# Performance work log

Measured on AMD Instinct MI355X. Metric: run time of the kernel, lower is better.

## Reference

```python
import jax, jax.numpy as jnp
import numpy as np

B, IN, H = 4096, 512, 1024
ALPHA, RHO = 0.001, 0.05

def setup_inputs() -> dict:
    key = jax.random.key(0)
    ks = jax.random.split(key, 9)
    inp = jax.random.normal(ks[0], (B, IN), dtype=jnp.float32)
    time = jax.random.uniform(ks[1], (B, 1), dtype=jnp.float32) * 100.0
    hx = jax.random.normal(ks[2], (B, H), dtype=jnp.float32)
    cx = jax.random.normal(ks[3], (B, H), dtype=jnp.float32)
    # params (match torch init scales loosely)
    Wxh_w = jax.random.normal(ks[4], (4 * H, IN), dtype=jnp.float32) / np.sqrt(IN)
    Wxh_b = jnp.zeros((4 * H,), dtype=jnp.float32)
    Whh_w = jax.random.normal(ks[5], (4 * H, H), dtype=jnp.float32) / np.sqrt(H)
    tau = jax.random.normal(ks[6], (H,), dtype=jnp.float32) * 0.5 + 5.0
    s = jax.random.uniform(ks[7], (H,), dtype=jnp.float32) * tau
    alpha = jnp.array([ALPHA], dtype=jnp.float32)
    rho = jnp.array([RHO], dtype=jnp.float32)
    return {"input": inp, "time": time, "hx": hx, "cx": cx,
            "Wxh_w": Wxh_w, "Wxh_b": Wxh_b, "Whh_w": Whh_w,
            "tau": tau, "s": s, "alpha": alpha, "rho": rho}

def _time_gate(time, s, tau, alpha, rho):
    # phi: [B, H] (time [B,1] broadcast against s/tau [H])
    phi = jnp.fmod(time - s, tau) / tau
    k = jnp.where(phi < rho / 2.0, 2.0 * phi / rho,
        jnp.where(phi < rho, 2.0 - 2.0 * phi / rho, alpha * phi))
    # computed under torch.no_grad() in the original
    return jax.lax.stop_gradient(k)

def reference(input, time, hx, cx, Wxh_w, Wxh_b, Whh_w, tau, s, alpha, rho):
    gates = input @ Wxh_w.T + Wxh_b + hx @ Whh_w.T  # [B, 4H]
    i, f, g, o = jnp.split(gates, 4, axis=1)
    k = _time_gate(time, s, tau, alpha, rho)
    ft = jax.nn.sigmoid(f + 1.0 - k)
    it = jax.nn.sigmoid(i) * k
    gt = jnp.tanh(g) * k
    ot = jax.nn.sigmoid(o) * k
    cy = ft * cx + it * gt
    hy = ot * jnp.tanh(cy)
    return (hy, cy)
```

## Files before the change

### kernel.cpp

```cpp
#include <hip/hip_runtime.h>

#define AS1 __attribute__((address_space(1)))
#define AS3 __attribute__((address_space(3)))

typedef _Float16 half_t;
typedef __attribute__((ext_vector_type(8))) _Float16 f16x8;
typedef __attribute__((ext_vector_type(4))) float f32x4;

static constexpr int Bsz = 4096;
static constexpr int INs = 512;
static constexpr int Hs  = 1024;
static constexpr int BM  = 128;
static constexpr int BH  = 32;
static constexpr int BK  = 64;
static constexpr int NIT = INs / BK + Hs / BK;

static constexpr size_t XN  = (size_t)Bsz * INs;
static constexpr size_t HXN = (size_t)Bsz * Hs;
static constexpr size_t WXN = (size_t)4 * Hs * INs;
static constexpr size_t WHN = (size_t)4 * Hs * Hs;
static constexpr size_t OFF_X  = 0;
static constexpr size_t OFF_HX = XN;
static constexpr size_t OFF_WX = XN + HXN;
static constexpr size_t OFF_WH = XN + HXN + WXN;
static constexpr size_t TOT    = XN + HXN + WXN + WHN;

__device__ __forceinline__ float sigm(float x) {
  return 1.0f / (1.0f + __expf(-x));
}
__device__ __forceinline__ float tanh_fast(float x) {
  const float e = __expf(2.0f * x);
  return 1.0f - 2.0f / (e + 1.0f);
}

__global__ __launch_bounds__(256)
void cvt_kernel(const float* __restrict__ x, const float* __restrict__ hx,
                const float* __restrict__ wx, const float* __restrict__ wh,
                half_t* __restrict__ ws) {
  const size_t cid = (size_t)blockIdx.x * 256 + threadIdx.x;
  const size_t e = cid * 8;
  const float* src; size_t off;
  if (e < OFF_HX)      { src = x;  off = e - OFF_X; }
  else if (e < OFF_WX) { src = hx; off = e - OFF_HX; }
  else if (e < OFF_WH) { src = wx; off = e - OFF_WX; }
  else                 { src = wh; off = e - OFF_WH; }
  const f32x4 a = *(const f32x4*)(src + off);
  const f32x4 b = *(const f32x4*)(src + off + 4);
  f16x8 o;
  o[0]=(half_t)a[0]; o[1]=(half_t)a[1]; o[2]=(half_t)a[2]; o[3]=(half_t)a[3];
  o[4]=(half_t)b[0]; o[5]=(half_t)b[1]; o[6]=(half_t)b[2]; o[7]=(half_t)b[3];
  *(f16x8*)(ws + e) = o;
}

__global__ __launch_bounds__(256, 4)
void plstm_gemm(const half_t* __restrict__ xin,
                const half_t* __restrict__ hxp,
                const float* __restrict__ cxp,
                const half_t* __restrict__ wxh,
                const float* __restrict__ biasp,
                const half_t* __restrict__ whh,
                const float* __restrict__ timep,
                const float* __restrict__ taup,
                const float* __restrict__ sp,
                const float* __restrict__ alphap,
                const float* __restrict__ rhop,
                float* __restrict__ outp)
{
  __shared__ half_t As[BM * BK];
  __shared__ half_t Bs[BM * BK];

  const int tid  = threadIdx.x;
  const int w    = tid >> 6;
  const int lane = tid & 63;
  const int l15  = lane & 15;
  const int grp  = lane >> 4;
  const int wr   = w >> 1;
  const int wc   = w & 1;

  const int m0 = blockIdx.x * BM;
  const int h0 = blockIdx.y * BH;

  f32x4 acc[4][4] = {};

  const int ldr = tid >> 3;
  const int ldc = tid & 7;

  for (int it = 0; it < NIT; ++it) {
    const bool p1 = it >= INs / BK;
    const half_t* Ap = p1 ? hxp : xin;
    const half_t* Wp = p1 ? whh : wxh;
    const int Ka = p1 ? Hs : INs;
    const int k0 = (p1 ? (it - INs / BK) : it) * BK;
    #pragma unroll
    for (int i = 0; i < 4; ++i) {
      const int e    = i * 32 + ldr;
      const int gc8  = ldc ^ (e & 7);
      const int wrow = ((e >> 4) & 3) * Hs + h0 + ((e >> 6) << 4) + (e & 15);
      const half_t* ga = Ap + (size_t)(m0 + e) * Ka + (k0 + gc8 * 8);
      __builtin_amdgcn_global_load_lds((AS1 void*)ga,
                                       (AS3 void*)(As + (e * 8 + ldc) * 8), 16, 0, 0);
      const half_t* gw = Wp + (size_t)wrow * Ka + (k0 + gc8 * 8);
      __builtin_amdgcn_global_load_lds((AS1 void*)gw,
                                       (AS3 void*)(Bs + (e * 8 + ldc) * 8), 16, 0, 0);
    }
    __syncthreads();

    #pragma unroll
    for (int kk = 0; kk < 2; ++kk) {
      const int c8x = kk * 4 + grp;
      f16x8 af[4], bfr[4];
      #pragma unroll
      for (int mt = 0; mt < 4; ++mt) {
        const int e = wr * 64 + mt * 16 + l15;
        af[mt] = *(const f16x8*)(As + (e * 8 + (c8x ^ (l15 & 7))) * 8);
      }
      #pragma unroll
      for (int nt = 0; nt < 4; ++nt) {
        const int e = wc * 64 + nt * 16 + l15;
        bfr[nt] = *(const f16x8*)(Bs + (e * 8 + (c8x ^ (l15 & 7))) * 8);
      }
      #pragma unroll
      for (int mt = 0; mt < 4; ++mt)
        #pragma unroll
        for (int nt = 0; nt < 4; ++nt)
          acc[mt][nt] = __builtin_amdgcn_mfma_f32_16x16x32_f16(
              af[mt], bfr[nt], acc[mt][nt], 0, 0, 0);
    }
    __syncthreads();
  }

  const int h = h0 + wc * 16 + l15;
  const float bi  = biasp[h];
  const float bfv = biasp[Hs + h];
  const float bg  = biasp[2 * Hs + h];
  const float bo  = biasp[3 * Hs + h];
  const float sv = sp[h], tauv = taup[h];
  const float alphav = alphap[0], rhov = rhop[0], rh = 0.5f * rhov;

  #pragma unroll
  for (int mt = 0; mt < 4; ++mt) {
    #pragma unroll
    for (int r = 0; r < 4; ++r) {
      const int brow = m0 + wr * 64 + mt * 16 + grp * 4 + r;
      const float tv = timep[brow];
      const float phi = fmodf(tv - sv, tauv) / tauv;
      float kv;
      if (phi < rh)        kv = (2.0f * phi) / rhov;
      else if (phi < rhov) kv = 2.0f - (2.0f * phi) / rhov;
      else                 kv = alphav * phi;

      const float iv = acc[mt][0][r] + bi;
      const float fv = acc[mt][1][r] + bfv;
      const float gv = acc[mt][2][r] + bg;
      const float ov = acc[mt][3][r] + bo;
      const float cxv = cxp[(size_t)brow * Hs + h];
      const float ft = sigm(fv + 1.0f - kv);
      const float it2 = sigm(iv) * kv;
      const float gt = tanh_fast(gv) * kv;
      const float ot = sigm(ov) * kv;
      const float cy = ft * cxv + it2 * gt;
      const float hy = ot * tanh_fast(cy);

      outp[(size_t)brow * Hs + h] = hy;
      outp[(size_t)Bsz * Hs + (size_t)brow * Hs + h] = cy;
    }
  }
}

__global__ __launch_bounds__(256, 3)
void plstm_gemm_f32(const float* __restrict__ xin, const float* __restrict__ timep,
                    const float* __restrict__ hxp, const float* __restrict__ cxp,
                    const float* __restrict__ wxh, const float* __restrict__ biasp,
                    const float* __restrict__ whh, const float* __restrict__ taup,
                    const float* __restrict__ sp, const float* __restrict__ alphap,
                    const float* __restrict__ rhop, float* __restrict__ outp)
{
  __shared__ half_t As[BM * BK];
  __shared__ half_t Bs[BM * BK];

  const int tid  = threadIdx.x;
  const int w    = tid >> 6;
  const int lane = tid & 63;
  const int l15  = lane & 15;
  const int grp  = lane >> 4;
  const int wr   = w >> 1;
  const int wc   = w & 1;

  const int m0 = blockIdx.x * BM;
  const int h0 = blockIdx.y * BH;

  f32x4 acc[4][4] = {};
  const int ldr = tid >> 3;
  const int ldc = tid & 7;

  for (int it = 0; it < NIT; ++it) {
    const bool p1 = it >= INs / BK;
    const float* Ap = p1 ? hxp : xin;
    const float* Wp = p1 ? whh : wxh;
    const int Ka = p1 ? Hs : INs;
    const int k0 = (p1 ? (it - INs / BK) : it) * BK;
    #pragma unroll
    for (int i = 0; i < 4; ++i) {
      const int e    = i * 32 + ldr;
      const int gc8  = ldc ^ (e & 7);
      const int wrow = ((e >> 4) & 3) * Hs + h0 + ((e >> 6) << 4) + (e & 15);
      const float* ga = Ap + (size_t)(m0 + e) * Ka + (k0 + gc8 * 8);
      const f32x4 a0 = *(const f32x4*)ga, a1 = *(const f32x4*)(ga + 4);
      f16x8 pa;
      pa[0]=(half_t)a0[0]; pa[1]=(half_t)a0[1]; pa[2]=(half_t)a0[2]; pa[3]=(half_t)a0[3];
      pa[4]=(half_t)a1[0]; pa[5]=(half_t)a1[1]; pa[6]=(half_t)a1[2]; pa[7]=(half_t)a1[3];
      *(f16x8*)(As + (e * 8 + ldc) * 8) = pa;
      const float* gw = Wp + (size_t)wrow * Ka + (k0 + gc8 * 8);
      const f32x4 b0 = *(const f32x4*)gw, b1 = *(const f32x4*)(gw + 4);
      f16x8 pb;
      pb[0]=(half_t)b0[0]; pb[1]=(half_t)b0[1]; pb[2]=(half_t)b0[2]; pb[3]=(half_t)b0[3];
      pb[4]=(half_t)b1[0]; pb[5]=(half_t)b1[1]; pb[6]=(half_t)b1[2]; pb[7]=(half_t)b1[3];
      *(f16x8*)(Bs + (e * 8 + ldc) * 8) = pb;
    }
    __syncthreads();
    #pragma unroll
    for (int kk = 0; kk < 2; ++kk) {
      const int c8x = kk * 4 + grp;
      f16x8 af[4], bfr[4];
      #pragma unroll
      for (int mt = 0; mt < 4; ++mt) {
        const int e = wr * 64 + mt * 16 + l15;
        af[mt] = *(const f16x8*)(As + (e * 8 + (c8x ^ (l15 & 7))) * 8);
      }
      #pragma unroll
      for (int nt = 0; nt < 4; ++nt) {
        const int e = wc * 64 + nt * 16 + l15;
        bfr[nt] = *(const f16x8*)(Bs + (e * 8 + (c8x ^ (l15 & 7))) * 8);
      }
      #pragma unroll
      for (int mt = 0; mt < 4; ++mt)
        #pragma unroll
        for (int nt = 0; nt < 4; ++nt)
          acc[mt][nt] = __builtin_amdgcn_mfma_f32_16x16x32_f16(
              af[mt], bfr[nt], acc[mt][nt], 0, 0, 0);
    }
    __syncthreads();
  }

  const int h = h0 + wc * 16 + l15;
  const float bi  = biasp[h];
  const float bfv = biasp[Hs + h];
  const float bg  = biasp[2 * Hs + h];
  const float bo  = biasp[3 * Hs + h];
  const float sv = sp[h], tauv = taup[h];
  const float alphav = alphap[0], rhov = rhop[0], rh = 0.5f * rhov;

  #pragma unroll
  for (int mt = 0; mt < 4; ++mt) {
    #pragma unroll
    for (int r = 0; r < 4; ++r) {
      const int brow = m0 + wr * 64 + mt * 16 + grp * 4 + r;
      const float tv = timep[brow];
      const float phi = fmodf(tv - sv, tauv) / tauv;
      float kv;
      if (phi < rh)        kv = (2.0f * phi) / rhov;
      else if (phi < rhov) kv = 2.0f - (2.0f * phi) / rhov;
      else                 kv = alphav * phi;
      const float iv = acc[mt][0][r] + bi;
      const float fv = acc[mt][1][r] + bfv;
      const float gv = acc[mt][2][r] + bg;
      const float ov = acc[mt][3][r] + bo;
      const float cxv = cxp[(size_t)brow * Hs + h];
      const float ft = sigm(fv + 1.0f - kv);
      const float it2 = sigm(iv) * kv;
      const float gt = tanh_fast(gv) * kv;
      const float ot = sigm(ov) * kv;
      const float cy = ft * cxv + it2 * gt;
      const float hy = ot * tanh_fast(cy);
      outp[(size_t)brow * Hs + h] = hy;
      outp[(size_t)Bsz * Hs + (size_t)brow * Hs + h] = cy;
    }
  }
}

extern "C" void kernel_launch(void* const* d_in, const int* in_sizes, int n_in,
                              void* d_out, int out_size, void* d_ws, size_t ws_size,
                              hipStream_t stream) {
  (void)in_sizes; (void)n_in; (void)out_size;
  const float* xin   = (const float*)d_in[0];
  const float* timep = (const float*)d_in[1];
  const float* hxp   = (const float*)d_in[2];
  const float* cxp   = (const float*)d_in[3];
  const float* wxh   = (const float*)d_in[4];
  const float* biasp = (const float*)d_in[5];
  const float* whh   = (const float*)d_in[6];
  const float* taup  = (const float*)d_in[7];
  const float* sp    = (const float*)d_in[8];
  const float* alphap= (const float*)d_in[9];
  const float* rhop  = (const float*)d_in[10];
  float* outp = (float*)d_out;

  dim3 grid(Bsz / BM, Hs / BH);
  if (ws_size >= TOT * sizeof(half_t)) {
    half_t* ws = (half_t*)d_ws;
    cvt_kernel<<<(int)(TOT / 8 / 256), 256, 0, stream>>>(xin, hxp, wxh, whh, ws);
    plstm_gemm<<<grid, 256, 0, stream>>>(
        ws + OFF_X, ws + OFF_HX, cxp, ws + OFF_WX, biasp, ws + OFF_WH,
        timep, taup, sp, alphap, rhop, outp);
  } else {
    plstm_gemm_f32<<<grid, 256, 0, stream>>>(
        xin, timep, hxp, cxp, wxh, biasp, whh,
        taup, sp, alphap, rhop, outp);
  }
}
```

Before: 193.5 us.

## Enlarge fp16 GEMM tile to 256x256 with double-buffered 8-wave pipelined schedule

Replaces the single-buffered 128x128-tile fp16 GEMM with a 256-row by 256-gate tile run by 512 threads. LDS is double-buffered and next-tile global_load_lds staging is interleaved with MFMA quadrants through explicit barriers, waitcnt and s_setprio phases. The aim is to overlap global loads with matrix math and raise arithmetic intensity per block. The risks are higher register pressure from the 8x4 accumulators, fewer blocks in flight, and correctness depending on the hand-placed vmcnt counts.

```diff
diff --git a/kernel.cpp b/kernel.cpp
--- a/kernel.cpp
+++ b/kernel.cpp
@@ -10,10 +10,11 @@
 static constexpr int Bsz = 4096;
 static constexpr int INs = 512;
 static constexpr int Hs  = 1024;
-static constexpr int BM  = 128;
-static constexpr int BH  = 32;
 static constexpr int BK  = 64;
 static constexpr int NIT = INs / BK + Hs / BK;
+
+static constexpr int BM  = 256;
+static constexpr int BHh = 64;
 
 static constexpr size_t XN  = (size_t)Bsz * INs;
 static constexpr size_t HXN = (size_t)Bsz * Hs;
@@ -52,7 +53,75 @@
   *(f16x8*)(ws + e) = o;
 }
 
-__global__ __launch_bounds__(256, 4)
+struct KS { const half_t* A; const half_t* W; int Ka; int k0; };
+
+
+#define STAGE_A(dst, s, mh) do { \
+  _Pragma("unroll") \
+  for (int rr = 0; rr < 2; ++rr) { \
+    const int e_ = rr * 128 + (mh) * 64 + j; \
+    const int gc8_ = ldc ^ (e_ & 7); \
+    const half_t* ga_ = (s).A + (size_t)(m0 + e_) * (s).Ka + ((s).k0 + gc8_ * 8); \
+    __builtin_amdgcn_global_load_lds((AS1 void*)ga_, \
+        (AS3 void*)((dst) + (e_ * 8 + ldc) * 8), 16, 0, 0); \
+  } } while (0)
+
+#define STAGE_B(dst, s, nh) do { \
+  _Pragma("unroll") \
+  for (int rr = 0; rr < 2; ++rr) { \
+    const int e_ = rr * 128 + ((j >> 5) << 6) + (nh) * 32 + (j & 31); \
+    const int gc8_ = ldc ^ (e_ & 7); \
+    const int wrow_ = ((e_ >> 4) & 3) * Hs + h0 + ((e_ >> 6) << 4) + (e_ & 15); \
+    const half_t* gw_ = (s).W + (size_t)wrow_ * (s).Ka + ((s).k0 + gc8_ * 8); \
+    __builtin_amdgcn_global_load_lds((AS1 void*)gw_, \
+        (AS3 void*)((dst) + (e_ * 8 + ldc) * 8), 16, 0, 0); \
+  } } while (0)
+
+#define READ_A(d, base, mh) do { \
+  _Pragma("unroll") \
+  for (int m_ = 0; m_ < 4; ++m_) { \
+    const int e_ = wr * 128 + (mh) * 64 + m_ * 16 + l15; \
+    _Pragma("unroll") \
+    for (int kk_ = 0; kk_ < 2; ++kk_) \
+      d[m_][kk_] = *(const f16x8*)((base) + (e_ * 8 + ((kk_ * 4 + grp) ^ (l15 & 7))) * 8); \
+  } } while (0)
+
+#define READ_B(d, base, nh) do { \
+  _Pragma("unroll") \
+  for (int n_ = 0; n_ < 2; ++n_) { \
+    const int e_ = wcn * 64 + (nh) * 32 + n_ * 16 + l15; \
+    _Pragma("unroll") \
+    for (int kk_ = 0; kk_ < 2; ++kk_) \
+      d[n_][kk_] = *(const f16x8*)((base) + (e_ * 8 + ((kk_ * 4 + grp) ^ (l15 & 7))) * 8); \
+  } } while (0)
+
+#define QUAD(mh, nh, A_, B_) do { \
+  _Pragma("unroll") \
+  for (int m_ = 0; m_ < 4; ++m_) \
+    _Pragma("unroll") \
+    for (int n_ = 0; n_ < 2; ++n_) \
+      _Pragma("unroll") \
+      for (int kk_ = 0; kk_ < 2; ++kk_) \
+        acc[(mh) * 4 + m_][(nh) * 2 + n_] = __builtin_amdgcn_mfma_f32_16x16x32_f16( \
+            A_[m_][kk_], B_[n_][kk_], acc[(mh) * 4 + m_][(nh) * 2 + n_], 0, 0, 0); \
+  } while (0)
+
+#define PH_MID() do { \
+  __builtin_amdgcn_s_barrier(); \
+  asm volatile("s_waitcnt lgkmcnt(0)" ::: "memory"); \
+  __builtin_amdgcn_sched_barrier(0); \
+  __builtin_amdgcn_s_setprio(1); } while (0)
+
+#define PH_END() do { \
+  __builtin_amdgcn_s_setprio(0); \
+  __builtin_amdgcn_s_barrier(); } while (0)
+
+#define PH_END_VM() do { \
+  __builtin_amdgcn_s_setprio(0); \
+  asm volatile("s_waitcnt vmcnt(4)" ::: "memory"); \
+  __builtin_amdgcn_s_barrier(); } while (0)
+
+__global__ __launch_bounds__(512, 2)
 void plstm_gemm(const half_t* __restrict__ xin,
                 const half_t* __restrict__ hxp,
                 const float* __restrict__ cxp,
@@ -66,70 +135,76 @@
                 const float* __restrict__ rhop,
                 float* __restrict__ outp)
 {
-  __shared__ half_t As[BM * BK];
-  __shared__ half_t Bs[BM * BK];
+  __shared__ half_t As[2][BM * BK];
+  __shared__ half_t Bs[2][BM * BK];
 
   const int tid  = threadIdx.x;
   const int w    = tid >> 6;
   const int lane = tid & 63;
   const int l15  = lane & 15;
   const int grp  = lane >> 4;
-  const int wr   = w >> 1;
-  const int wc   = w & 1;
+  const int wr   = w >> 2;
+  const int wcn  = w & 3;
 
   const int m0 = blockIdx.x * BM;
-  const int h0 = blockIdx.y * BH;
-
-  f32x4 acc[4][4] = {};
-
-  const int ldr = tid >> 3;
+  const int h0 = blockIdx.y * BHh;
+
+  const int j   = tid >> 3;
   const int ldc = tid & 7;
 
-  for (int it = 0; it < NIT; ++it) {
-    const bool p1 = it >= INs / BK;
-    const half_t* Ap = p1 ? hxp : xin;
-    const half_t* Wp = p1 ? whh : wxh;
-    const int Ka = p1 ? Hs : INs;
-    const int k0 = (p1 ? (it - INs / BK) : it) * BK;
-    #pragma unroll
-    for (int i = 0; i < 4; ++i) {
-      const int e    = i * 32 + ldr;
-      const int gc8  = ldc ^ (e & 7);
-      const int wrow = ((e >> 4) & 3) * Hs + h0 + ((e >> 6) << 4) + (e & 15);
-      const half_t* ga = Ap + (size_t)(m0 + e) * Ka + (k0 + gc8 * 8);
-      __builtin_amdgcn_global_load_lds((AS1 void*)ga,
-                                       (AS3 void*)(As + (e * 8 + ldc) * 8), 16, 0, 0);
-      const half_t* gw = Wp + (size_t)wrow * Ka + (k0 + gc8 * 8);
-      __builtin_amdgcn_global_load_lds((AS1 void*)gw,
-                                       (AS3 void*)(Bs + (e * 8 + ldc) * 8), 16, 0, 0);
-    }
-    __syncthreads();
-
-    #pragma unroll
-    for (int kk = 0; kk < 2; ++kk) {
-      const int c8x = kk * 4 + grp;
-      f16x8 af[4], bfr[4];
-      #pragma unroll
-      for (int mt = 0; mt < 4; ++mt) {
-        const int e = wr * 64 + mt * 16 + l15;
-        af[mt] = *(const f16x8*)(As + (e * 8 + (c8x ^ (l15 & 7))) * 8);
-      }
-      #pragma unroll
-      for (int nt = 0; nt < 4; ++nt) {
-        const int e = wc * 64 + nt * 16 + l15;
-        bfr[nt] = *(const f16x8*)(Bs + (e * 8 + (c8x ^ (l15 & 7))) * 8);
-      }
-      #pragma unroll
-      for (int mt = 0; mt < 4; ++mt)
-        #pragma unroll
-        for (int nt = 0; nt < 4; ++nt)
-          acc[mt][nt] = __builtin_amdgcn_mfma_f32_16x16x32_f16(
-              af[mt], bfr[nt], acc[mt][nt], 0, 0, 0);
-    }
-    __syncthreads();
-  }
-
-  const int h = h0 + wc * 16 + l15;
+  f32x4 acc[8][4] = {};
+  f16x8 a0[4][2], a1[4][2], b0[2][2], b1[2][2];
+
+  auto ks = [&](int t) -> KS {
+    if (t >= NIT) t -= NIT;
+    KS r;
+    if (t < INs / BK) { r.A = xin; r.W = wxh; r.Ka = INs; r.k0 = t * BK; }
+    else              { r.A = hxp; r.W = whh; r.Ka = Hs;  r.k0 = (t - INs / BK) * BK; }
+    return r;
+  };
+
+  {
+    const KS s0 = ks(0), s1 = ks(1);
+    STAGE_A(As[0], s0, 0); STAGE_A(As[0], s0, 1);
+    STAGE_B(Bs[0], s0, 0); STAGE_B(Bs[0], s0, 1);
+    STAGE_B(Bs[1], s1, 0); STAGE_A(As[1], s1, 1);
+    asm volatile("s_waitcnt vmcnt(4)" ::: "memory");
+    __builtin_amdgcn_s_barrier();
+  }
+
+  #pragma unroll 1
+  for (int i = 0; i < NIT / 2; ++i) {
+    const int t0 = 2 * i;
+    const KS k1 = ks(t0 + 1), k2 = ks(t0 + 2), k3 = ks(t0 + 3);
+
+    READ_A(a0, As[0], 0); READ_B(b0, Bs[0], 0);
+    STAGE_A(As[1], k1, 0);
+    PH_MID(); QUAD(0, 0, a0, b0); PH_END();
+    READ_A(a1, As[0], 1);
+    STAGE_B(Bs[1], k1, 1);
+    PH_MID(); QUAD(1, 0, a1, b0); PH_END();
+    READ_B(b1, Bs[0], 1);
+    STAGE_B(Bs[0], k2, 0);
+    PH_MID(); QUAD(1, 1, a1, b1); PH_END();
+    READ_A(a0, As[0], 0);
+    STAGE_A(As[0], k2, 1);
+    PH_MID(); QUAD(0, 1, a0, b1); PH_END_VM();
+
+    READ_A(a0, As[1], 0); READ_B(b0, Bs[1], 0);
+    STAGE_A(As[0], k2, 0);
+    PH_MID(); QUAD(0, 0, a0, b0); PH_END();
+    READ_A(a1, As[1], 1);
+    STAGE_B(Bs[0], k2, 1);
+    PH_MID(); QUAD(1, 0, a1, b0); PH_END();
+    READ_B(b1, Bs[1], 1);
+    STAGE_B(Bs[1], k3, 0);
+    PH_MID(); QUAD(1, 1, a1, b1); PH_END();
+    READ_A(a0, As[1], 0);
+    STAGE_A(As[1], k3, 1);
+    PH_MID(); QUAD(0, 1, a0, b1); PH_END_VM();
+  }
+
+  const int h = h0 + wcn * 16 + l15;
   const float bi  = biasp[h];
   const float bfv = biasp[Hs + h];
   const float bg  = biasp[2 * Hs + h];
@@ -138,10 +213,10 @@
   const float alphav = alphap[0], rhov = rhop[0], rh = 0.5f * rhov;
 
   #pragma unroll
-  for (int mt = 0; mt < 4; ++mt) {
+  for (int mt = 0; mt < 8; ++mt) {
     #pragma unroll
     for (int r = 0; r < 4; ++r) {
-      const int brow = m0 + wr * 64 + mt * 16 + grp * 4 + r;
+      const int brow = m0 + wr * 128 + mt * 16 + grp * 4 + r;
       const float tv = timep[brow];
       const float phi = fmodf(tv - sv, tauv) / tauv;
       float kv;
@@ -175,19 +250,19 @@
                     const float* __restrict__ sp, const float* __restrict__ alphap,
                     const float* __restrict__ rhop, float* __restrict__ outp)
 {
-  __shared__ half_t As[BM * BK];
-  __shared__ half_t Bs[BM * BK];
+  __shared__ half_t Asf[128 * BK];
+  __shared__ half_t Bsf[128 * BK];
 
   const int tid  = threadIdx.x;
   const int w    = tid >> 6;
   const int lane = tid & 63;
   const int l15  = lane & 15;
   const int grp  = lane >> 4;
-  const int wr   = w >> 1;
-  const int wc   = w & 1;
-
-  const int m0 = blockIdx.x * BM;
-  const int h0 = blockIdx.y * BH;
+  const int wrl  = w >> 1;
+  const int wcl  = w & 1;
+
+  const int m0 = blockIdx.x * 128;
+  const int h0 = blockIdx.y * 32;
 
   f32x4 acc[4][4] = {};
   const int ldr = tid >> 3;
@@ -205,17 +280,17 @@
       const int gc8  = ldc ^ (e & 7);
       const int wrow = ((e >> 4) & 3) * Hs + h0 + ((e >> 6) << 4) + (e & 15);
       const float* ga = Ap + (size_t)(m0 + e) * Ka + (k0 + gc8 * 8);
-      const f32x4 a0 = *(const f32x4*)ga, a1 = *(const f32x4*)(ga + 4);
+      const f32x4 a0v = *(const f32x4*)ga, a1v = *(const f32x4*)(ga + 4);
       f16x8 pa;
-      pa[0]=(half_t)a0[0]; pa[1]=(half_t)a0[1]; pa[2]=(half_t)a0[2]; pa[3]=(half_t)a0[3];
-      pa[4]=(half_t)a1[0]; pa[5]=(half_t)a1[1]; pa[6]=(half_t)a1[2]; pa[7]=(half_t)a1[3];
-      *(f16x8*)(As + (e * 8 + ldc) * 8) = pa;
+      pa[0]=(half_t)a0v[0]; pa[1]=(half_t)a0v[1]; pa[2]=(half_t)a0v[2]; pa[3]=(half_t)a0v[3];
+      pa[4]=(half_t)a1v[0]; pa[5]=(half_t)a1v[1]; pa[6]=(half_t)a1v[2]; pa[7]=(half_t)a1v[3];
+      *(f16x8*)(Asf + (e * 8 + ldc) * 8) = pa;
       const float* gw = Wp + (size_t)wrow * Ka + (k0 + gc8 * 8);
-      const f32x4 b0 = *(const f32x4*)gw, b1 = *(const f32x4*)(gw + 4);
+      const f32x4 b0v = *(const f32x4*)gw, b1v = *(const f32x4*)(gw + 4);
       f16x8 pb;
-      pb[0]=(half_t)b0[0]; pb[1]=(half_t)b0[1]; pb[2]=(half_t)b0[2]; pb[3]=(half_t)b0[3];
-      pb[4]=(half_t)b1[0]; pb[5]=(half_t)b1[1]; pb[6]=(half_t)b1[2]; pb[7]=(half_t)b1[3];
-      *(f16x8*)(Bs + (e * 8 + ldc) * 8) = pb;
+      pb[0]=(half_t)b0v[0]; pb[1]=(half_t)b0v[1]; pb[2]=(half_t)b0v[2]; pb[3]=(half_t)b0v[3];
+      pb[4]=(half_t)b1v[0]; pb[5]=(half_t)b1v[1]; pb[6]=(half_t)b1v[2]; pb[7]=(half_t)b1v[3];
+      *(f16x8*)(Bsf + (e * 8 + ldc) * 8) = pb;
     }
     __syncthreads();
     #pragma unroll
@@ -224,13 +299,13 @@
       f16x8 af[4], bfr[4];
       #pragma unroll
       for (int mt = 0; mt < 4; ++mt) {
-        const int e = wr * 64 + mt * 16 + l15;
-        af[mt] = *(const f16x8*)(As + (e * 8 + (c8x ^ (l15 & 7))) * 8);
+        const int e = wrl * 64 + mt * 16 + l15;
+        af[mt] = *(const f16x8*)(Asf + (e * 8 + (c8x ^ (l15 & 7))) * 8);
       }
       #pragma unroll
       for (int nt = 0; nt < 4; ++nt) {
-        const int e = wc * 64 + nt * 16 + l15;
-        bfr[nt] = *(const f16x8*)(Bs + (e * 8 + (c8x ^ (l15 & 7))) * 8);
+        const int e = wcl * 64 + nt * 16 + l15;
+        bfr[nt] = *(const f16x8*)(Bsf + (e * 8 + (c8x ^ (l15 & 7))) * 8);
       }
       #pragma unroll
       for (int mt = 0; mt < 4; ++mt)
@@ -242,7 +317,7 @@
     __syncthreads();
   }
 
-  const int h = h0 + wc * 16 + l15;
+  const int h = h0 + wcl * 16 + l15;
   const float bi  = biasp[h];
   const float bfv = biasp[Hs + h];
   const float bg  = biasp[2 * Hs + h];
@@ -254,7 +329,7 @@
   for (int mt = 0; mt < 4; ++mt) {
     #pragma unroll
     for (int r = 0; r < 4; ++r) {
-      const int brow = m0 + wr * 64 + mt * 16 + grp * 4 + r;
+      const int brow = m0 + wrl * 64 + mt * 16 + grp * 4 + r;
       const float tv = timep[brow];
       const float phi = fmodf(tv - sv, tauv) / tauv;
       float kv;
@@ -295,15 +370,16 @@
   const float* rhop  = (const float*)d_in[10];
   float* outp = (float*)d_out;
 
-  dim3 grid(Bsz / BM, Hs / BH);
   if (ws_size >= TOT * sizeof(half_t)) {
     half_t* ws = (half_t*)d_ws;
     cvt_kernel<<<(int)(TOT / 8 / 256), 256, 0, stream>>>(xin, hxp, wxh, whh, ws);
-    plstm_gemm<<<grid, 256, 0, stream>>>(
+    dim3 grid(Bsz / BM, Hs / BHh);
+    plstm_gemm<<<grid, 512, 0, stream>>>(
         ws + OFF_X, ws + OFF_HX, cxp, ws + OFF_WX, biasp, ws + OFF_WH,
         timep, taup, sp, alphap, rhop, outp);
   } else {
-    plstm_gemm_f32<<<grid, 256, 0, stream>>>(
+    dim3 fgrid(Bsz / 128, Hs / 32);
+    plstm_gemm_f32<<<fgrid, 256, 0, stream>>>(
         xin, timep, hxp, cxp, wxh, biasp, whh,
         taup, sp, alphap, rhop, outp);
   }
```

Measured after the change: 195.1 us. No clear change (+0.8%).
